# Performance work log

Hardware: AMD Instinct MI355X
Metric: run time of the kernel (lower is better)

Reference implementation:

```python
import jax, jax.numpy as jnp
import numpy as np

B, S, H, NH = 2, 2048, 768, 12
HD = H // NH  # 64
MAXPOS = 2048


def _rope_tables(max_pos, d):
    # bert4torch get_sinusoid_encoding_table: even cols sin, odd cols cos
    pos = np.arange(max_pos, dtype=np.float32)[:, None]
    div = np.exp(np.arange(0, d, 2, dtype=np.float32) * (-np.log(10000.0) / d))
    tab = np.zeros((max_pos, d), np.float32)
    tab[:, 0::2] = np.sin(pos * div)
    tab[:, 1::2] = np.cos(pos * div)
    cos = np.concatenate([tab[:, 1::2], tab[:, 1::2]], axis=1)  # [:,1::2].repeat(1,2)
    sin = np.concatenate([tab[:, 0::2], tab[:, 0::2]], axis=1)  # [:,0::2].repeat(1,2)
    return jnp.asarray(cos), jnp.asarray(sin)


def setup_inputs() -> dict:
    key = jax.random.key(0)
    ks = jax.random.split(key, 10)
    s = 0.02
    inp = {}
    inp["hidden_states"] = jax.random.normal(ks[0], (B, S, H), jnp.float32)
    inp["attention_mask"] = jnp.ones((B, 1, 1, S), jnp.float32)
    for i, n in enumerate(["q", "k", "v", "o"]):
        inp[f"W{n}"] = (jax.random.normal(ks[1 + i], (H, H), jnp.float32) * s)
        inp[f"b{n}"] = jnp.zeros((H,), jnp.float32)
    cos, sin = _rope_tables(MAXPOS, HD)
    inp["cos_position"] = cos
    inp["sin_position"] = sin
    return inp


def _apply_rope(qw, cos, sin):
    # Faithful to source: seq_len_dim defaults to 1, which on a
    # [B, heads, S, head_dim] tensor is the HEADS axis.
    L = qw.shape[1]
    qw2 = jnp.concatenate([-qw[..., 1::2], qw[..., 0::2]], axis=-1)
    return qw * cos[:L][None, :, None, :] + qw2 * sin[:L][None, :, None, :]


def reference(hidden_states, attention_mask, Wq, bq, Wk, bk, Wv, bv, Wo, bo,
              cos_position, sin_position):
    b, s, _ = hidden_states.shape

    def heads(x):  # [b,s,H] -> [b,NH,s,HD]
        return x.reshape(b, s, NH, HD).transpose(0, 2, 1, 3)

    q = heads(hidden_states @ Wq + bq)
    k = heads(hidden_states @ Wk + bk)
    v = heads(hidden_states @ Wv + bv)
    q = _apply_rope(q, cos_position, sin_position)
    k = _apply_rope(k, cos_position, sin_position)
    scores = jnp.einsum('bnid,bnjd->bnij', q, k) / jnp.sqrt(jnp.float32(HD))
    scores = scores + (1.0 - attention_mask) * (-10000.0)
    probs = jax.nn.softmax(scores, axis=-1)  # dropout is identity in eval
    ctx = jnp.einsum('bnij,bnjd->bnid', probs, v)
    ctx = ctx.transpose(0, 2, 1, 3).reshape(b, s, H)
    return ctx @ Wo + bo
```

## Files before the change

### kernel.cpp

```cpp
#include <hip/hip_runtime.h>

#define B 2
#define S 2048
#define H 768
#define NH 12
#define HD 64
#define BS (B * S)
#define LOG2E 1.4426950408889634f

typedef unsigned short u16;
typedef unsigned int u32;
typedef short short8 __attribute__((ext_vector_type(8)));
typedef float f32x4 __attribute__((ext_vector_type(4)));
typedef float f32x16 __attribute__((ext_vector_type(16)));

__device__ __forceinline__ u16 f2bf(float f) {
    union { float f; unsigned u; } c; c.f = f;
    unsigned u = c.u + 0x7FFFu + ((c.u >> 16) & 1u);
    return (u16)(u >> 16);
}
__device__ __forceinline__ float bf2f(u16 h) {
    union { unsigned u; float f; } c; c.u = ((unsigned)h) << 16;
    return c.f;
}
__device__ __forceinline__ f32x16 zero16() {
    f32x16 v;
    #pragma unroll
    for (int i = 0; i < 16; ++i) v[i] = 0.f;
    return v;
}
union pk4 { uint4 u; short8 s; };

__device__ __forceinline__ void g2l16(const u16* g, u16* l) {
    __builtin_amdgcn_global_load_lds(
        (const __attribute__((address_space(1))) void*)g,
        (__attribute__((address_space(3))) void*)l, 16, 0, 0);
}

__global__ __launch_bounds__(256) void prep_kernel(
    const float* __restrict__ hs,
    const float* __restrict__ Wq, const float* __restrict__ Wk,
    const float* __restrict__ Wv, const float* __restrict__ Wo,
    const float* __restrict__ bq, const float* __restrict__ bk,
    const float* __restrict__ cosp, const float* __restrict__ sinp,
    u16* __restrict__ hsb, u16* __restrict__ WTqkv, u16* __restrict__ WTo,
    float* __restrict__ bqk2)
{
    __shared__ float Lt[64 * 65];
    const int bid = blockIdx.x;
    const int t = threadIdx.x;

    if (bid >= 576) {
        size_t i = ((size_t)(bid - 576) * 256 + t) * 8;
        float4 a = *(const float4*)(hs + i);
        float4 b = *(const float4*)(hs + i + 4);
        short8 p;
        p[0] = (short)f2bf(a.x); p[1] = (short)f2bf(a.y);
        p[2] = (short)f2bf(a.z); p[3] = (short)f2bf(a.w);
        p[4] = (short)f2bf(b.x); p[5] = (short)f2bf(b.y);
        p[6] = (short)f2bf(b.z); p[7] = (short)f2bf(b.w);
        *(short8*)(hsb + i) = p;
        return;
    }

    const int z   = bid / 144;
    const int rem = bid - z * 144;
    const int k0 = (rem / 12) * 64, n0 = (rem % 12) * 64;
    const float* W = (z == 0) ? Wq : (z == 1) ? Wk : (z == 2) ? Wv : Wo;
    u16* D = (z == 3) ? WTo : (WTqkv + (size_t)z * H * H);
    const int head = n0 >> 6;
    const float scl = (z == 0) ? (0.125f * LOG2E) : 1.0f;

    if (z < 2 && rem / 12 == 0 && t < 64) {
        const float* bs = (z == 0) ? bq : bk;
        int d = t;
        int pd = (d < 32) ? (2 * d + 1) : (2 * (d - 32));
        float sv = ((d < 32) ? -1.f : 1.f) * sinp[head * HD + d];
        float cv = cosp[head * HD + d];
        bqk2[z * H + n0 + d] = scl * (cv * bs[n0 + d] + sv * bs[n0 + pd]);
    }

    #pragma unroll
    for (int u = 0; u < 4; ++u) {
        int f = t + u * 256;
        int r = f >> 4, c4 = (f & 15) * 4;
        float4 w = *(const float4*)(W + (size_t)(k0 + r) * H + n0 + c4);
        Lt[r * 65 + c4 + 0] = w.x; Lt[r * 65 + c4 + 1] = w.y;
        Lt[r * 65 + c4 + 2] = w.z; Lt[r * 65 + c4 + 3] = w.w;
    }
    __syncthreads();
    #pragma unroll
    for (int u = 0; u < 4; ++u) {
        int f = t + u * 256;
        int n = f >> 4, k4 = (f & 15) * 4;
        ushort4 p;
        if (z < 2) {
            int pn = (n < 32) ? (2 * n + 1) : (2 * (n - 32));
            float cv = scl * cosp[head * HD + n];
            float sv = scl * ((n < 32) ? -1.f : 1.f) * sinp[head * HD + n];
            p.x = f2bf(cv * Lt[(k4 + 0) * 65 + n] + sv * Lt[(k4 + 0) * 65 + pn]);
            p.y = f2bf(cv * Lt[(k4 + 1) * 65 + n] + sv * Lt[(k4 + 1) * 65 + pn]);
            p.z = f2bf(cv * Lt[(k4 + 2) * 65 + n] + sv * Lt[(k4 + 2) * 65 + pn]);
            p.w = f2bf(cv * Lt[(k4 + 3) * 65 + n] + sv * Lt[(k4 + 3) * 65 + pn]);
        } else {
            p.x = f2bf(Lt[(k4 + 0) * 65 + n]);
            p.y = f2bf(Lt[(k4 + 1) * 65 + n]);
            p.z = f2bf(Lt[(k4 + 2) * 65 + n]);
            p.w = f2bf(Lt[(k4 + 3) * 65 + n]);
        }
        *(ushort4*)(D + (size_t)(n0 + n) * H + k0 + k4) = p;
    }
}

__global__ __launch_bounds__(256) void gemm_qkv_kernel(
    const u16* __restrict__ A, const u16* __restrict__ BT,
    const float* __restrict__ bqk2, const float* __restrict__ bv,
    u16* __restrict__ Qb, u16* __restrict__ Kb, u16* __restrict__ VT)
{
    __shared__ alignas(16) u16 Abuf[2][128 * 64];
    __shared__ alignas(16) u16 Bbuf[2][128 * 64];

    const int tid  = threadIdx.x;
    const int w    = tid >> 6;
    const int lane = tid & 63;
    const int quad = lane >> 4;
    const int l15  = lane & 15;
    const int wm = (w & 1) * 64, wn = (w >> 1) * 64;
    const int m0 = (blockIdx.x & 31) * 128;
    const int n0 = (blockIdx.x >> 5) * 128;
    const int NK = H / 64;

    int srow[4], slc[4];
    #pragma unroll
    for (int u = 0; u < 4; ++u) {
        int s = u * 256 + tid;
        srow[u] = s >> 3;
        slc[u]  = (s & 7) ^ (srow[u] & 7);
    }

    #define QSTAGE(IT, NB)                                                    \
        _Pragma("unroll")                                                     \
        for (int u = 0; u < 4; ++u) {                                         \
            g2l16(A  + (size_t)(m0 + srow[u]) * H + (IT) * 64 + slc[u] * 8,   \
                  &Abuf[NB][(u * 256 + w * 64) * 8]);                         \
            g2l16(BT + (size_t)(n0 + srow[u]) * H + (IT) * 64 + slc[u] * 8,   \
                  &Bbuf[NB][(u * 256 + w * 64) * 8]);                         \
        }

    QSTAGE(0, 0)

    f32x4 acc[4][4];
    #pragma unroll
    for (int i = 0; i < 4; ++i)
        #pragma unroll
        for (int j = 0; j < 4; ++j) acc[i][j] = (f32x4){0.f, 0.f, 0.f, 0.f};

    for (int it = 0; it < NK; ++it) {
        const int cur = it & 1;
        __syncthreads();
        if (it + 1 < NK) { QSTAGE(it + 1, cur ^ 1) }

        const u16* Ac = Abuf[cur];
        const u16* Bc = Bbuf[cur];
        #pragma unroll
        for (int kc = 0; kc < 2; ++kc) {
            const int ch = kc * 4 + quad;
            short8 af[4], bf[4];
            #pragma unroll
            for (int mi = 0; mi < 4; ++mi) {
                int row = wm + mi * 16 + l15;
                af[mi] = *(const short8*)&Ac[row * 64 + (ch ^ (row & 7)) * 8];
            }
            #pragma unroll
            for (int ni = 0; ni < 4; ++ni) {
                int row = wn + ni * 16 + l15;
                bf[ni] = *(const short8*)&Bc[row * 64 + (ch ^ (row & 7)) * 8];
            }
            #pragma unroll
            for (int mi = 0; mi < 4; ++mi)
                #pragma unroll
                for (int ni = 0; ni < 4; ++ni)
                    acc[mi][ni] = __builtin_amdgcn_mfma_f32_16x16x32_bf16(
                        af[mi], bf[ni], acc[mi][ni], 0, 0, 0);
        }
    }
    #undef QSTAGE

    #pragma unroll
    for (int mi = 0; mi < 4; ++mi) {
        const int mbase = m0 + wm + mi * 16 + quad * 4;
        #pragma unroll
        for (int ni = 0; ni < 4; ++ni) {
            const int col = n0 + wn + ni * 16 + l15;
            const int which = col / H;
            const int c = col - which * H;
            const int h = c >> 6, d = c & 63;
            if (which == 2) {
                const float bias = bv[c];
                const int b_ = mbase >> 11, s = mbase & (S - 1);
                ushort4 pk;
                pk.x = f2bf(acc[mi][ni][0] + bias);
                pk.y = f2bf(acc[mi][ni][1] + bias);
                pk.z = f2bf(acc[mi][ni][2] + bias);
                pk.w = f2bf(acc[mi][ni][3] + bias);
                *(ushort4*)&VT[(((size_t)b_ * NH + h) * HD + d) * S + s] = pk;
            } else {
                u16* dst = (which == 0) ? Qb : Kb;
                const float bias = bqk2[which * H + c];
                #pragma unroll
                for (int r = 0; r < 4; ++r) {
                    int m = mbase + r;
                    int b_ = m >> 11, s = m & (S - 1);
                    dst[(((size_t)b_ * NH + h) * S + s) * HD + d] =
                        f2bf(acc[mi][ni][r] + bias);
                }
            }
        }
    }
}

__global__ __launch_bounds__(256) void gemm_out_kernel(
    const u16* __restrict__ A, const u16* __restrict__ BT,
    const float* __restrict__ bo, float* __restrict__ out)
{
    __shared__ alignas(16) u16 Abuf[2][128 * 64];
    __shared__ alignas(16) u16 Bbuf[2][64 * 64];

    const int tid  = threadIdx.x;
    const int w    = tid >> 6;
    const int lane = tid & 63;
    const int quad = lane >> 4;
    const int l15  = lane & 15;
    const int wm = (w & 1) * 64, wn = (w >> 1) * 32;
    const int m0 = (blockIdx.x & 31) * 128;
    const int n0 = (blockIdx.x >> 5) * 64;
    const int NK = H / 64;

    int srow[4], slc[4];
    #pragma unroll
    for (int u = 0; u < 4; ++u) {
        int s = u * 256 + tid;
        srow[u] = s >> 3;
        slc[u]  = (s & 7) ^ (srow[u] & 7);
    }

    #define OSTAGE(IT, NB)                                                    \
        _Pragma("unroll")                                                     \
        for (int u = 0; u < 4; ++u)                                           \
            g2l16(A + (size_t)(m0 + srow[u]) * H + (IT) * 64 + slc[u] * 8,    \
                  &Abuf[NB][(u * 256 + w * 64) * 8]);                         \
        _Pragma("unroll")                                                     \
        for (int u = 0; u < 2; ++u)                                           \
            g2l16(BT + (size_t)(n0 + srow[u]) * H + (IT) * 64 + slc[u] * 8,   \
                  &Bbuf[NB][(u * 256 + w * 64) * 8]);

    OSTAGE(0, 0)

    f32x4 acc[4][2];
    #pragma unroll
    for (int i = 0; i < 4; ++i)
        #pragma unroll
        for (int j = 0; j < 2; ++j) acc[i][j] = (f32x4){0.f, 0.f, 0.f, 0.f};

    for (int it = 0; it < NK; ++it) {
        const int cur = it & 1;
        __syncthreads();
        if (it + 1 < NK) { OSTAGE(it + 1, cur ^ 1) }

        const u16* Ac = Abuf[cur];
        const u16* Bc = Bbuf[cur];
        #pragma unroll
        for (int kc = 0; kc < 2; ++kc) {
            const int ch = kc * 4 + quad;
            short8 af[4], bf[2];
            #pragma unroll
            for (int mi = 0; mi < 4; ++mi) {
                int row = wm + mi * 16 + l15;
                af[mi] = *(const short8*)&Ac[row * 64 + (ch ^ (row & 7)) * 8];
            }
            #pragma unroll
            for (int ni = 0; ni < 2; ++ni) {
                int row = wn + ni * 16 + l15;
                bf[ni] = *(const short8*)&Bc[row * 64 + (ch ^ (row & 7)) * 8];
            }
            #pragma unroll
            for (int mi = 0; mi < 4; ++mi)
                #pragma unroll
                for (int ni = 0; ni < 2; ++ni)
                    acc[mi][ni] = __builtin_amdgcn_mfma_f32_16x16x32_bf16(
                        af[mi], bf[ni], acc[mi][ni], 0, 0, 0);
        }
    }
    #undef OSTAGE

    #pragma unroll
    for (int mi = 0; mi < 4; ++mi) {
        const int mbase = m0 + wm + mi * 16 + quad * 4;
        #pragma unroll
        for (int ni = 0; ni < 2; ++ni) {
            const int col = n0 + wn + ni * 16 + l15;
            const float bias = bo[col];
            #pragma unroll
            for (int r = 0; r < 4; ++r)
                out[(size_t)(mbase + r) * H + col] = acc[mi][ni][r] + bias;
        }
    }
}

__global__ __launch_bounds__(256) void attn_mfma_kernel(
    const u16* __restrict__ Q, const u16* __restrict__ K,
    const u16* __restrict__ VT, const float* __restrict__ mask,
    u16* __restrict__ ctx)
{
    __shared__ alignas(16) u16 smem[21504];
    u16* const Kbase = smem;
    u16* const Vbase = smem + 8192;

    const int tid  = threadIdx.x;
    const int w    = tid >> 6;
    const int lane = tid & 63;
    const int l31  = lane & 31;
    const int h5   = lane >> 5;
    const int rh   = w & 1;
    const int kh   = w >> 1;
    const int bid = blockIdx.x;
    const int bn = bid % 24;
    const int q0 = (bid / 24) * 64;
    const int b = bn / NH, hh = bn % NH;
    const int NT = S / 64;

    short8 qa[4];
    {
        const u16* Qp = Q + ((size_t)bn * S + q0 + rh * 32 + l31) * HD + h5 * 8;
        #pragma unroll
        for (int kc = 0; kc < 4; ++kc)
            qa[kc] = *(const short8*)(Qp + kc * 16);
    }

    short8 oneb = {};
    if (h5 == 0) oneb[0] = (short)0x3F80;

    const u16* Kg = K + (size_t)bn * S * HD;
    const u16* Vg = VT + (size_t)bn * HD * S;
    const float* mrow = mask + (size_t)b * S;

    int srow[2], slc[2];
    #pragma unroll
    for (int u = 0; u < 2; ++u) {
        int s = u * 256 + tid;
        srow[u] = s >> 3;
        slc[u]  = (s & 7) ^ (srow[u] & 7);
    }

    #define STAGE(JT, NB)                                                     \
        _Pragma("unroll")                                                     \
        for (int u = 0; u < 2; ++u) {                                         \
            g2l16(Kg + (size_t)((JT) * 64 + srow[u]) * HD + slc[u] * 8,       \
                  Kbase + (NB) * 4096 + (u * 256 + w * 64) * 8);              \
            g2l16(Vg + (size_t)srow[u] * S + (JT) * 64 + slc[u] * 8,          \
                  Vbase + (NB) * 4096 + (u * 256 + w * 64) * 8);              \
        }

    STAGE(0, 0)

    f32x16 o0 = zero16(), o1 = zero16();
    float l_acc = 0.f;

    for (int jt = 0; jt < NT; ++jt) {
        const int cur = jt & 1;
        const float mv = mrow[jt * 64 + kh * 32 + l31];
        __syncthreads();
        if (jt + 1 < NT) { STAGE(jt + 1, cur ^ 1) }

        const u16* Kc = Kbase + cur * 4096;
        const u16* Vc = Vbase + cur * 4096;

        const float mt = (1.0f - mv) * (-10000.0f * LOG2E);
        short8 mta = {};
        if (h5 == 0) mta[0] = (short)f2bf(mt);
        f32x16 sc = __builtin_amdgcn_mfma_f32_32x32x16_bf16(
            mta, oneb, zero16(), 0, 0, 0);

        {
            const int krow = kh * 32 + l31;
            const int sw = krow & 7;
            #pragma unroll
            for (int kc = 0; kc < 4; ++kc) {
                const short8 kb =
                    *(const short8*)&Kc[krow * 64 + ((kc * 2 + h5) ^ sw) * 8];
                sc = __builtin_amdgcn_mfma_f32_32x32x16_bf16(kb, qa[kc], sc, 0, 0, 0);
            }
        }

        short8 va[2][2];
        #pragma unroll
        for (int nt = 0; nt < 2; ++nt) {
            const int vrow = nt * 32 + l31;
            const int sw = vrow & 7;
            va[nt][0] = *(const short8*)&Vc[vrow * 64 + ((kh * 4 + h5) ^ sw) * 8];
            va[nt][1] = *(const short8*)&Vc[vrow * 64 + ((kh * 4 + 2 + h5) ^ sw) * 8];
        }

        float p[16];
        #pragma unroll
        for (int r = 0; r < 16; ++r) {
            p[r] = __builtin_amdgcn_exp2f(sc[r]);
            l_acc += p[r];
        }
        u32 d[8];
        #pragma unroll
        for (int i = 0; i < 8; ++i)
            d[i] = ((u32)f2bf(p[2 * i + 1]) << 16) | (u32)f2bf(p[2 * i]);

        u32 e0 = h5 ? d[0] : d[2];
        u32 e1 = h5 ? d[1] : d[3];
        u32 e2 = h5 ? d[4] : d[6];
        u32 e3 = h5 ? d[5] : d[7];
        u32 r0 = (u32)__shfl_xor((int)e0, 32, 64);
        u32 r1 = (u32)__shfl_xor((int)e1, 32, 64);
        u32 r2 = (u32)__shfl_xor((int)e2, 32, 64);
        u32 r3 = (u32)__shfl_xor((int)e3, 32, 64);

        pk4 f0, f1;
        if (h5) {
            f0.u = make_uint4(r0, r1, d[2], d[3]);
            f1.u = make_uint4(r2, r3, d[6], d[7]);
        } else {
            f0.u = make_uint4(d[0], d[1], r0, r1);
            f1.u = make_uint4(d[4], d[5], r2, r3);
        }

        o0 = __builtin_amdgcn_mfma_f32_32x32x16_bf16(va[0][0], f0.s, o0, 0, 0, 0);
        o0 = __builtin_amdgcn_mfma_f32_32x32x16_bf16(va[0][1], f1.s, o0, 0, 0, 0);
        o1 = __builtin_amdgcn_mfma_f32_32x32x16_bf16(va[1][0], f0.s, o1, 0, 0, 0);
        o1 = __builtin_amdgcn_mfma_f32_32x32x16_bf16(va[1][1], f1.s, o1, 0, 0, 0);
    }
    #undef STAGE

    l_acc += __shfl_xor(l_acc, 32, 64);

    __syncthreads();
    float* cb = (float*)smem;
    float* lb = (float*)(smem + 16384);

    if (kh == 1) {
        #pragma unroll
        for (int r = 0; r < 16; ++r) {
            cb[r * 128 + rh * 64 + lane]        = o0[r];
            cb[(16 + r) * 128 + rh * 64 + lane] = o1[r];
        }
        if (h5 == 0) lb[rh * 32 + l31] = l_acc;
    }
    __syncthreads();
    if (kh == 0) {
        float lt = l_acc + lb[rh * 32 + l31];
        float inv = 1.0f / lt;
        const int s = q0 + rh * 32 + l31;
        u16* dst = ctx + ((size_t)b * S + s) * H + hh * 64;
        #pragma unroll
        for (int g = 0; g < 4; ++g) {
            ushort4 pk0, pk1;
            pk0.x = f2bf((o0[4 * g + 0] + cb[(4 * g + 0) * 128 + rh * 64 + lane]) * inv);
            pk0.y = f2bf((o0[4 * g + 1] + cb[(4 * g + 1) * 128 + rh * 64 + lane]) * inv);
            pk0.z = f2bf((o0[4 * g + 2] + cb[(4 * g + 2) * 128 + rh * 64 + lane]) * inv);
            pk0.w = f2bf((o0[4 * g + 3] + cb[(4 * g + 3) * 128 + rh * 64 + lane]) * inv);
            *(ushort4*)(dst + 8 * g + 4 * h5) = pk0;
            pk1.x = f2bf((o1[4 * g + 0] + cb[(16 + 4 * g + 0) * 128 + rh * 64 + lane]) * inv);
            pk1.y = f2bf((o1[4 * g + 1] + cb[(16 + 4 * g + 1) * 128 + rh * 64 + lane]) * inv);
            pk1.z = f2bf((o1[4 * g + 2] + cb[(16 + 4 * g + 2) * 128 + rh * 64 + lane]) * inv);
            pk1.w = f2bf((o1[4 * g + 3] + cb[(16 + 4 * g + 3) * 128 + rh * 64 + lane]) * inv);
            *(ushort4*)(dst + 32 + 8 * g + 4 * h5) = pk1;
        }
    }
}

extern "C" void kernel_launch(void* const* d_in, const int* in_sizes, int n_in,
                              void* d_out, int out_size, void* d_ws, size_t ws_size,
                              hipStream_t stream)
{
    const float* hs   = (const float*)d_in[0];
    const float* mask = (const float*)d_in[1];
    const float* Wq   = (const float*)d_in[2];
    const float* bq   = (const float*)d_in[3];
    const float* Wk   = (const float*)d_in[4];
    const float* bk   = (const float*)d_in[5];
    const float* Wv   = (const float*)d_in[6];
    const float* bv   = (const float*)d_in[7];
    const float* Wo   = (const float*)d_in[8];
    const float* bo   = (const float*)d_in[9];
    const float* cosp = (const float*)d_in[10];
    const float* sinp = (const float*)d_in[11];
    float* out = (float*)d_out;

    const size_t per = (size_t)B * NH * S * HD;
    u16* ws    = (u16*)d_ws;
    u16* hsb   = ws;
    u16* WTqkv = hsb + per;
    u16* WTo   = WTqkv + (size_t)3 * H * H;
    u16* Qb    = WTo + (size_t)H * H;
    u16* Kb    = Qb + per;
    u16* VT    = Kb + per;
    u16* ctxb  = VT + per;
    float* bqk2 = (float*)(ctxb + per);

    prep_kernel<<<576 + (BS * H) / 2048, 256, 0, stream>>>(
        hs, Wq, Wk, Wv, Wo, bq, bk, cosp, sinp, hsb, WTqkv, WTo, bqk2);

    gemm_qkv_kernel<<<(BS / 128) * (2304 / 128), 256, 0, stream>>>(
        hsb, WTqkv, bqk2, bv, Qb, Kb, VT);

    attn_mfma_kernel<<<(S / 64) * (B * NH), 256, 0, stream>>>(
        Qb, Kb, VT, mask, ctxb);

    gemm_out_kernel<<<(BS / 128) * (H / 64), 256, 0, stream>>>(
        ctxb, WTo, bo, out);
}
```

Before: 189.9 us.

## Use permlane32 swap and MFMA row-sum, shrink LDS for higher occupancy

Result: faster. 185.6 us (-2.3%).

```diff
diff --git a/kernel.cpp b/kernel.cpp
--- a/kernel.cpp
+++ b/kernel.cpp
@@ -307,12 +307,12 @@
     }
 }
 
-__global__ __launch_bounds__(256) void attn_mfma_kernel(
+__global__ __launch_bounds__(256, 4) void attn_mfma_kernel(
     const u16* __restrict__ Q, const u16* __restrict__ K,
     const u16* __restrict__ VT, const float* __restrict__ mask,
     u16* __restrict__ ctx)
 {
-    __shared__ alignas(16) u16 smem[21504];
+    __shared__ alignas(16) u16 smem[16384];
     u16* const Kbase = smem;
     u16* const Vbase = smem + 8192;
 
@@ -340,6 +340,10 @@
     short8 oneb = {};
     if (h5 == 0) oneb[0] = (short)0x3F80;
 
+    short8 onesa;
+    #pragma unroll
+    for (int i = 0; i < 8; ++i) onesa[i] = (short)0x3F80;
+
     const u16* Kg = K + (size_t)bn * S * HD;
     const u16* Vg = VT + (size_t)bn * HD * S;
     const float* mrow = mask + (size_t)b * S;
@@ -363,8 +367,7 @@
 
     STAGE(0, 0)
 
-    f32x16 o0 = zero16(), o1 = zero16();
-    float l_acc = 0.f;
+    f32x16 o0 = zero16(), o1 = zero16(), lac = zero16();
 
     for (int jt = 0; jt < NT; ++jt) {
         const int cur = jt & 1;
@@ -403,45 +406,40 @@
 
         float p[16];
         #pragma unroll
-        for (int r = 0; r < 16; ++r) {
+        for (int r = 0; r < 16; ++r)
             p[r] = __builtin_amdgcn_exp2f(sc[r]);
-            l_acc += p[r];
-        }
         u32 d[8];
         #pragma unroll
         for (int i = 0; i < 8; ++i)
             d[i] = ((u32)f2bf(p[2 * i + 1]) << 16) | (u32)f2bf(p[2 * i]);
 
-        u32 e0 = h5 ? d[0] : d[2];
-        u32 e1 = h5 ? d[1] : d[3];
-        u32 e2 = h5 ? d[4] : d[6];
-        u32 e3 = h5 ? d[5] : d[7];
-        u32 r0 = (u32)__shfl_xor((int)e0, 32, 64);
-        u32 r1 = (u32)__shfl_xor((int)e1, 32, 64);
-        u32 r2 = (u32)__shfl_xor((int)e2, 32, 64);
-        u32 r3 = (u32)__shfl_xor((int)e3, 32, 64);
+        u32 a0 = d[0], b0 = d[2];
+        u32 a1 = d[1], b1 = d[3];
+        u32 a2 = d[4], b2 = d[6];
+        u32 a3 = d[5], b3 = d[7];
+        asm("v_permlane32_swap_b32 %0, %1" : "+v"(a0), "+v"(b0));
+        asm("v_permlane32_swap_b32 %0, %1" : "+v"(a1), "+v"(b1));
+        asm("v_permlane32_swap_b32 %0, %1" : "+v"(a2), "+v"(b2));
+        asm("v_permlane32_swap_b32 %0, %1" : "+v"(a3), "+v"(b3));
 
         pk4 f0, f1;
-        if (h5) {
-            f0.u = make_uint4(r0, r1, d[2], d[3]);
-            f1.u = make_uint4(r2, r3, d[6], d[7]);
-        } else {
-            f0.u = make_uint4(d[0], d[1], r0, r1);
-            f1.u = make_uint4(d[4], d[5], r2, r3);
-        }
+        f0.u = make_uint4(a0, a1, b0, b1);
+        f1.u = make_uint4(a2, a3, b2, b3);
 
         o0 = __builtin_amdgcn_mfma_f32_32x32x16_bf16(va[0][0], f0.s, o0, 0, 0, 0);
         o0 = __builtin_amdgcn_mfma_f32_32x32x16_bf16(va[0][1], f1.s, o0, 0, 0, 0);
         o1 = __builtin_amdgcn_mfma_f32_32x32x16_bf16(va[1][0], f0.s, o1, 0, 0, 0);
         o1 = __builtin_amdgcn_mfma_f32_32x32x16_bf16(va[1][1], f1.s, o1, 0, 0, 0);
+        lac = __builtin_amdgcn_mfma_f32_32x32x16_bf16(onesa, f0.s, lac, 0, 0, 0);
+        lac = __builtin_amdgcn_mfma_f32_32x32x16_bf16(onesa, f1.s, lac, 0, 0, 0);
     }
     #undef STAGE
 
-    l_acc += __shfl_xor(l_acc, 32, 64);
+    float l_acc = lac[0];
 
     __syncthreads();
     float* cb = (float*)smem;
-    float* lb = (float*)(smem + 16384);
+    float* lb = (float*)(smem + 8192);
 
     if (kh == 1) {
         #pragma unroll
```
